# Performance work log

Measured on AMD Instinct MI355X. Metric: run time of the kernel, lower is better.

The kernel has to match this reference:

```python
import jax, jax.numpy as jnp
import numpy as np


def _edt(mask_zero):
    """Exact 2D Euclidean distance transform: distance of every pixel to the
    nearest True pixel in mask_zero (matches scipy.ndimage.distance_transform_edt
    applied to the one-hot map, where background pixels are zeros).
    mask_zero: [B, C, H, W] bool, True where the one-hot map is 0.
    Returns float32 [B, C, H, W].
    """
    B, C, H, W = mask_zero.shape
    BIG = jnp.float32(H + W)  # larger than any in-image 1D distance

    # Phase 1: 1D distance to nearest zero along axis H (forward + backward scans)
    def step(d, m):  # d,m: [B, C, W]
        d = jnp.where(m, 0.0, d + 1.0)
        return d, d

    m_rows = jnp.moveaxis(mask_zero, 2, 0)  # [H, B, C, W]
    init = jnp.full((B, C, W), BIG, dtype=jnp.float32)
    _, g_f = jax.lax.scan(step, init, m_rows)
    _, g_b = jax.lax.scan(step, init, m_rows[::-1])
    g = jnp.minimum(g_f, g_b[::-1])          # [H, B, C, W]
    g = jnp.moveaxis(g, 0, 2)                # [B, C, H, W]

    # Phase 2: exact combine along axis W: d2[.., i, j] = min_k g[.., i, k]^2 + (j-k)^2
    j = jnp.arange(W, dtype=jnp.float32)
    sq = (j[:, None] - j[None, :]) ** 2      # [W(j), W(k)]
    d2 = jnp.min(g[..., None, :] ** 2 + sq, axis=-1)  # [B, C, H, W]
    return jnp.sqrt(d2)


def _rrwmap(y_, num_classes):
    labels = y_[:, 0]  # [B, H, W]
    # one-hot channel c is zero where label != c
    mask_zero = labels[:, None, :, :] != jnp.arange(num_classes)[None, :, None, None]
    d = _edt(mask_zero)                                  # [B, C, H, W]
    maxd = jnp.max(d, axis=(2, 3), keepdims=True)        # per (b, c) max
    rrw = -(d / (maxd + 1e-15))
    return jnp.where(rrw == 0.0, 1.0, rrw)


def setup_inputs() -> dict:
    key = jax.random.key(0)
    k1, k2 = jax.random.split(key)
    B, C, H, W = 2, 4, 256, 256
    x = jax.random.normal(k1, (B, C, H, W), dtype=jnp.float32)
    y_ = jax.random.randint(k2, (B, 1, H, W), 0, C, dtype=jnp.int64)
    return {"x": x, "y_": y_}


def reference(x, y_):
    C = x.shape[1]
    rrw = _rrwmap(y_, C)
    p = jax.nn.softmax(x, axis=1)
    return jnp.mean(p * rrw)
```

## Files before the change

kernel.cpp:

```cpp
#include <hip/hip_runtime.h>

#define B_ 2
#define C_ 4
#define H_ 256
#define W_ 256
constexpr int BC    = B_ * C_;
constexpr int HW    = H_ * W_;
constexpr int NROWS = B_ * H_;
constexpr int NTOT  = B_ * C_ * HW;
constexpr float BIGF = (float)(H_ + W_);
constexpr int PF    = 6;

__global__ __launch_bounds__(256) void rows_kernel(
    const int* __restrict__ lab, const float* __restrict__ x,
    float* __restrict__ ps4, float* __restrict__ pm4, float* __restrict__ pa) {
    const int r = blockIdx.x;
    const int b = r >> 8;
    const int i = r & (H_ - 1);
    const int j = threadIdx.x;

    const int* lrow = lab + b * HW + i * W_;
    const int  c    = lrow[j];

    const float* xp = x + b * C_ * HW + i * W_ + j;
    const float x0 = xp[0 * HW], x1 = xp[1 * HW], x2 = xp[2 * HW], x3 = xp[3 * HW];

    const int* lcol = lab + b * HW + j;
    int lu[PF + 1], ld[PF + 1];
    #pragma unroll
    for (int k = 1; k <= PF; ++k) {
        const int ru = i - k, rd = i + k;
        lu[k] = lcol[(ru >= 0 ? ru : 0) * W_];
        ld[k] = lcol[(rd < H_ ? rd : H_ - 1) * W_];
    }
    float gu = -1.0f, gd = -1.0f;
    #pragma unroll
    for (int k = 1; k <= PF; ++k) {
        if (gu < 0.0f) {
            if (i - k < 0) gu = BIGF + (float)(i + 1);
            else if (lu[k] != c) gu = (float)k;
        }
        if (gd < 0.0f) {
            if (i + k >= H_) gd = BIGF + (float)(H_ - i);
            else if (ld[k] != c) gd = (float)k;
        }
    }
    for (int k = PF + 1; gu < 0.0f || gd < 0.0f; ++k) {
        if (gu < 0.0f) {
            const int rr = i - k;
            if (rr < 0) gu = BIGF + (float)(i + 1);
            else if (lcol[rr * W_] != c) gu = (float)k;
        }
        if (gd < 0.0f) {
            const int rr = i + k;
            if (rr >= H_) gd = BIGF + (float)(H_ - i);
            else if (lcol[rr * W_] != c) gd = (float)k;
        }
    }
    const float g = fminf(gu, gd);

    __shared__ int   ls[W_];
    __shared__ float g2s[W_];
    ls[j]  = c;
    g2s[j] = g * g;
    __syncthreads();

    float best = g * g;
    for (int dj = 1; dj < W_; ++dj) {
        const float dd = (float)(dj * dj);
        if (dd >= best) break;
        const int l = j - dj, rr = j + dj;
        if (l >= 0) {
            const float v = (ls[l] == c ? g2s[l] : 0.0f) + dd;
            best = fminf(best, v);
        }
        if (rr < W_) {
            const float v = (ls[rr] == c ? g2s[rr] : 0.0f) + dd;
            best = fminf(best, v);
        }
    }

    const float mx = fmaxf(fmaxf(x0, x1), fmaxf(x2, x3));
    const float e0 = __expf(x0 - mx), e1 = __expf(x1 - mx);
    const float e2 = __expf(x2 - mx), e3 = __expf(x3 - mx);
    const float s  = e0 + e1 + e2 + e3;
    const float ec = (c == 0) ? e0 : (c == 1) ? e1 : (c == 2) ? e2 : e3;
    const float pc = ec / s;

    float va = (s - ec) / s;
    const float psv = pc * sqrtf(best);
    float s0 = (c == 0) ? psv : 0.0f, s1 = (c == 1) ? psv : 0.0f;
    float s2 = (c == 2) ? psv : 0.0f, s3 = (c == 3) ? psv : 0.0f;
    float m0 = (c == 0) ? best : 0.0f, m1 = (c == 1) ? best : 0.0f;
    float m2 = (c == 2) ? best : 0.0f, m3 = (c == 3) ? best : 0.0f;

    #pragma unroll
    for (int off = 32; off; off >>= 1) {
        va += __shfl_down(va, off, 64);
        s0 += __shfl_down(s0, off, 64);
        s1 += __shfl_down(s1, off, 64);
        s2 += __shfl_down(s2, off, 64);
        s3 += __shfl_down(s3, off, 64);
        m0 = fmaxf(m0, __shfl_down(m0, off, 64));
        m1 = fmaxf(m1, __shfl_down(m1, off, 64));
        m2 = fmaxf(m2, __shfl_down(m2, off, 64));
        m3 = fmaxf(m3, __shfl_down(m3, off, 64));
    }
    __shared__ float lred[4][9];
    const int lane = j & 63, wid = j >> 6;
    if (lane == 0) {
        lred[wid][0] = va;
        lred[wid][1] = s0; lred[wid][2] = s1; lred[wid][3] = s2; lred[wid][4] = s3;
        lred[wid][5] = m0; lred[wid][6] = m1; lred[wid][7] = m2; lred[wid][8] = m3;
    }
    __syncthreads();
    if (j == 0) {
        float A = 0.0f, S0 = 0.0f, S1 = 0.0f, S2 = 0.0f, S3 = 0.0f;
        float M0 = 0.0f, M1 = 0.0f, M2 = 0.0f, M3 = 0.0f;
        #pragma unroll
        for (int w = 0; w < 4; ++w) {
            A  += lred[w][0];
            S0 += lred[w][1]; S1 += lred[w][2]; S2 += lred[w][3]; S3 += lred[w][4];
            M0 = fmaxf(M0, lred[w][5]); M1 = fmaxf(M1, lred[w][6]);
            M2 = fmaxf(M2, lred[w][7]); M3 = fmaxf(M3, lred[w][8]);
        }
        ((float4*)ps4)[r] = make_float4(S0, S1, S2, S3);
        ((float4*)pm4)[r] = make_float4(M0, M1, M2, M3);
        pa[r] = A;
    }
}

__global__ __launch_bounds__(64) void final_kernel(
    const float4* __restrict__ ps4, const float4* __restrict__ pm4,
    const float* __restrict__ pa, float* __restrict__ out) {
    const int t = threadIdx.x;
    float a = 0.0f;
    float4 sb0 = make_float4(0.f, 0.f, 0.f, 0.f), sb1 = sb0;
    float4 mb0 = sb0, mb1 = sb0;
    #pragma unroll
    for (int q = 0; q < 4; ++q) {
        const int r0 = t + q * 64;
        const int r1 = r0 + 256;
        a += pa[r0] + pa[r1];
        float4 v;
        v = ps4[r0]; sb0.x += v.x; sb0.y += v.y; sb0.z += v.z; sb0.w += v.w;
        v = ps4[r1]; sb1.x += v.x; sb1.y += v.y; sb1.z += v.z; sb1.w += v.w;
        v = pm4[r0]; mb0.x = fmaxf(mb0.x, v.x); mb0.y = fmaxf(mb0.y, v.y);
                     mb0.z = fmaxf(mb0.z, v.z); mb0.w = fmaxf(mb0.w, v.w);
        v = pm4[r1]; mb1.x = fmaxf(mb1.x, v.x); mb1.y = fmaxf(mb1.y, v.y);
                     mb1.z = fmaxf(mb1.z, v.z); mb1.w = fmaxf(mb1.w, v.w);
    }
    #pragma unroll
    for (int off = 32; off; off >>= 1) {
        a     += __shfl_down(a, off, 64);
        sb0.x += __shfl_down(sb0.x, off, 64); sb0.y += __shfl_down(sb0.y, off, 64);
        sb0.z += __shfl_down(sb0.z, off, 64); sb0.w += __shfl_down(sb0.w, off, 64);
        sb1.x += __shfl_down(sb1.x, off, 64); sb1.y += __shfl_down(sb1.y, off, 64);
        sb1.z += __shfl_down(sb1.z, off, 64); sb1.w += __shfl_down(sb1.w, off, 64);
        mb0.x = fmaxf(mb0.x, __shfl_down(mb0.x, off, 64));
        mb0.y = fmaxf(mb0.y, __shfl_down(mb0.y, off, 64));
        mb0.z = fmaxf(mb0.z, __shfl_down(mb0.z, off, 64));
        mb0.w = fmaxf(mb0.w, __shfl_down(mb0.w, off, 64));
        mb1.x = fmaxf(mb1.x, __shfl_down(mb1.x, off, 64));
        mb1.y = fmaxf(mb1.y, __shfl_down(mb1.y, off, 64));
        mb1.z = fmaxf(mb1.z, __shfl_down(mb1.z, off, 64));
        mb1.w = fmaxf(mb1.w, __shfl_down(mb1.w, off, 64));
    }
    if (t == 0) {
        float total = a;
        total -= sb0.x / (sqrtf(mb0.x) + 1e-15f);
        total -= sb0.y / (sqrtf(mb0.y) + 1e-15f);
        total -= sb0.z / (sqrtf(mb0.z) + 1e-15f);
        total -= sb0.w / (sqrtf(mb0.w) + 1e-15f);
        total -= sb1.x / (sqrtf(mb1.x) + 1e-15f);
        total -= sb1.y / (sqrtf(mb1.y) + 1e-15f);
        total -= sb1.z / (sqrtf(mb1.z) + 1e-15f);
        total -= sb1.w / (sqrtf(mb1.w) + 1e-15f);
        out[0] = total / (float)NTOT;
    }
}

extern "C" void kernel_launch(void* const* d_in, const int* in_sizes, int n_in,
                              void* d_out, int out_size, void* d_ws, size_t ws_size,
                              hipStream_t stream) {
    const float* x = (const float*)d_in[0];
    const int*   y = (const int*)d_in[1];
    float* out = (float*)d_out;

    float* ps4 = (float*)d_ws;
    float* pm4 = ps4 + NROWS * 4;
    float* pa  = pm4 + NROWS * 4;

    rows_kernel<<<NROWS, W_, 0, stream>>>(y, x, ps4, pm4, pa);
    final_kernel<<<1, 64, 0, stream>>>((const float4*)ps4, (const float4*)pm4, pa, out);
}
```

Before: 61.72 us.

## Process four pixels per thread with vectorized int4/float4 loads, single-wavefront blocks

Each block now uses one 64-lane wavefront, and each thread handles four adjacent columns using int4/float4 loads for labels and logits. Because the block is a single wavefront, the cross-wave shared-memory reduction and its second barrier go away. The prefetch depth for the vertical scan grows from 6 to 8 rows. The trade-off is less parallelism: four times fewer threads overall, and each thread runs four serial horizontal EDT searches plus four vertical fallback loops, which adds latency and divergence.

```diff
diff --git a/kernel.cpp b/kernel.cpp
--- a/kernel.cpp
+++ b/kernel.cpp
@@ -9,90 +9,124 @@
 constexpr int NROWS = B_ * H_;
 constexpr int NTOT  = B_ * C_ * HW;
 constexpr float BIGF = (float)(H_ + W_);
-constexpr int PF    = 6;
-
-__global__ __launch_bounds__(256) void rows_kernel(
+constexpr int PF    = 8;
+
+__device__ __forceinline__ int   icomp(const int4& v, int p) {
+    return p == 0 ? v.x : p == 1 ? v.y : p == 2 ? v.z : v.w;
+}
+__device__ __forceinline__ float fcomp(const float4& v, int p) {
+    return p == 0 ? v.x : p == 1 ? v.y : p == 2 ? v.z : v.w;
+}
+
+__global__ __launch_bounds__(64) void rows_kernel(
     const int* __restrict__ lab, const float* __restrict__ x,
     float* __restrict__ ps4, float* __restrict__ pm4, float* __restrict__ pa) {
     const int r = blockIdx.x;
     const int b = r >> 8;
     const int i = r & (H_ - 1);
-    const int j = threadIdx.x;
-
-    const int* lrow = lab + b * HW + i * W_;
-    const int  c    = lrow[j];
-
-    const float* xp = x + b * C_ * HW + i * W_ + j;
-    const float x0 = xp[0 * HW], x1 = xp[1 * HW], x2 = xp[2 * HW], x3 = xp[3 * HW];
-
-    const int* lcol = lab + b * HW + j;
-    int lu[PF + 1], ld[PF + 1];
+    const int t = threadIdx.x;
+
+    const int4* lrowv = (const int4*)(lab + b * HW + i * W_);
+    const int4  L     = lrowv[t];
+
+    const float4* xv = (const float4*)(x + b * C_ * HW + i * W_) + t;
+    const float4 X0 = xv[0 * (HW / 4)], X1 = xv[1 * (HW / 4)];
+    const float4 X2 = xv[2 * (HW / 4)], X3 = xv[3 * (HW / 4)];
+
+    const int4* lcolv = (const int4*)(lab + b * HW) + t;
+    int4 lu[PF + 1], ld[PF + 1];
     #pragma unroll
     for (int k = 1; k <= PF; ++k) {
         const int ru = i - k, rd = i + k;
-        lu[k] = lcol[(ru >= 0 ? ru : 0) * W_];
-        ld[k] = lcol[(rd < H_ ? rd : H_ - 1) * W_];
-    }
-    float gu = -1.0f, gd = -1.0f;
+        lu[k] = lcolv[(ru >= 0 ? ru : 0) * (W_ / 4)];
+        ld[k] = lcolv[(rd < H_ ? rd : H_ - 1) * (W_ / 4)];
+    }
+
+    float gu[4], gd[4];
+    #pragma unroll
+    for (int p = 0; p < 4; ++p) { gu[p] = -1.0f; gd[p] = -1.0f; }
     #pragma unroll
     for (int k = 1; k <= PF; ++k) {
-        if (gu < 0.0f) {
-            if (i - k < 0) gu = BIGF + (float)(i + 1);
-            else if (lu[k] != c) gu = (float)k;
-        }
-        if (gd < 0.0f) {
-            if (i + k >= H_) gd = BIGF + (float)(H_ - i);
-            else if (ld[k] != c) gd = (float)k;
-        }
-    }
-    for (int k = PF + 1; gu < 0.0f || gd < 0.0f; ++k) {
-        if (gu < 0.0f) {
+        #pragma unroll
+        for (int p = 0; p < 4; ++p) {
+            const int cp = icomp(L, p);
+            if (gu[p] < 0.0f) {
+                if (i - k < 0) gu[p] = BIGF + (float)(i + 1);
+                else if (icomp(lu[k], p) != cp) gu[p] = (float)k;
+            }
+            if (gd[p] < 0.0f) {
+                if (i + k >= H_) gd[p] = BIGF + (float)(H_ - i);
+                else if (icomp(ld[k], p) != cp) gd[p] = (float)k;
+            }
+        }
+    }
+    #pragma unroll
+    for (int p = 0; p < 4; ++p) {
+        const int* lcolp = lab + b * HW + 4 * t + p;
+        const int  cp    = icomp(L, p);
+        for (int k = PF + 1; gu[p] < 0.0f; ++k) {
             const int rr = i - k;
-            if (rr < 0) gu = BIGF + (float)(i + 1);
-            else if (lcol[rr * W_] != c) gu = (float)k;
-        }
-        if (gd < 0.0f) {
+            if (rr < 0) gu[p] = BIGF + (float)(i + 1);
+            else if (lcolp[rr * W_] != cp) gu[p] = (float)k;
+        }
+        for (int k = PF + 1; gd[p] < 0.0f; ++k) {
             const int rr = i + k;
-            if (rr >= H_) gd = BIGF + (float)(H_ - i);
-            else if (lcol[rr * W_] != c) gd = (float)k;
-        }
-    }
-    const float g = fminf(gu, gd);
-
-    __shared__ int   ls[W_];
-    __shared__ float g2s[W_];
-    ls[j]  = c;
-    g2s[j] = g * g;
+            if (rr >= H_) gd[p] = BIGF + (float)(H_ - i);
+            else if (lcolp[rr * W_] != cp) gd[p] = (float)k;
+        }
+    }
+
+    __shared__ alignas(16) int   ls[W_];
+    __shared__ alignas(16) float g2s[W_];
+    float g2[4];
+    #pragma unroll
+    for (int p = 0; p < 4; ++p) {
+        const float g = fminf(gu[p], gd[p]);
+        g2[p] = g * g;
+    }
+    ((int4*)ls)[t]    = L;
+    ((float4*)g2s)[t] = make_float4(g2[0], g2[1], g2[2], g2[3]);
     __syncthreads();
 
-    float best = g * g;
-    for (int dj = 1; dj < W_; ++dj) {
-        const float dd = (float)(dj * dj);
-        if (dd >= best) break;
-        const int l = j - dj, rr = j + dj;
-        if (l >= 0) {
-            const float v = (ls[l] == c ? g2s[l] : 0.0f) + dd;
-            best = fminf(best, v);
-        }
-        if (rr < W_) {
-            const float v = (ls[rr] == c ? g2s[rr] : 0.0f) + dd;
-            best = fminf(best, v);
-        }
-    }
-
-    const float mx = fmaxf(fmaxf(x0, x1), fmaxf(x2, x3));
-    const float e0 = __expf(x0 - mx), e1 = __expf(x1 - mx);
-    const float e2 = __expf(x2 - mx), e3 = __expf(x3 - mx);
-    const float s  = e0 + e1 + e2 + e3;
-    const float ec = (c == 0) ? e0 : (c == 1) ? e1 : (c == 2) ? e2 : e3;
-    const float pc = ec / s;
-
-    float va = (s - ec) / s;
-    const float psv = pc * sqrtf(best);
-    float s0 = (c == 0) ? psv : 0.0f, s1 = (c == 1) ? psv : 0.0f;
-    float s2 = (c == 2) ? psv : 0.0f, s3 = (c == 3) ? psv : 0.0f;
-    float m0 = (c == 0) ? best : 0.0f, m1 = (c == 1) ? best : 0.0f;
-    float m2 = (c == 2) ? best : 0.0f, m3 = (c == 3) ? best : 0.0f;
+    float best[4];
+    #pragma unroll
+    for (int p = 0; p < 4; ++p) {
+        const int j  = 4 * t + p;
+        const int cp = icomp(L, p);
+        float bb = g2[p];
+        for (int dj = 1; dj < W_; ++dj) {
+            const float dd = (float)(dj * dj);
+            if (dd >= bb) break;
+            const int l = j - dj, rr = j + dj;
+            if (l >= 0)  bb = fminf(bb, (ls[l] == cp ? g2s[l] : 0.0f) + dd);
+            if (rr < W_) bb = fminf(bb, (ls[rr] == cp ? g2s[rr] : 0.0f) + dd);
+        }
+        best[p] = bb;
+    }
+
+    float va = 0.0f;
+    float s0 = 0.0f, s1 = 0.0f, s2 = 0.0f, s3 = 0.0f;
+    float m0 = 0.0f, m1 = 0.0f, m2 = 0.0f, m3 = 0.0f;
+    #pragma unroll
+    for (int p = 0; p < 4; ++p) {
+        const float x0 = fcomp(X0, p), x1 = fcomp(X1, p);
+        const float x2 = fcomp(X2, p), x3 = fcomp(X3, p);
+        const float mx = fmaxf(fmaxf(x0, x1), fmaxf(x2, x3));
+        const float e0 = __expf(x0 - mx), e1 = __expf(x1 - mx);
+        const float e2 = __expf(x2 - mx), e3 = __expf(x3 - mx);
+        const float s  = e0 + e1 + e2 + e3;
+        const int   cp = icomp(L, p);
+        const float ec = (cp == 0) ? e0 : (cp == 1) ? e1 : (cp == 2) ? e2 : e3;
+        const float pc = ec / s;
+        va += (s - ec) / s;
+        const float psv = pc * sqrtf(best[p]);
+        s0 += (cp == 0) ? psv : 0.0f; s1 += (cp == 1) ? psv : 0.0f;
+        s2 += (cp == 2) ? psv : 0.0f; s3 += (cp == 3) ? psv : 0.0f;
+        m0 = fmaxf(m0, (cp == 0) ? best[p] : 0.0f);
+        m1 = fmaxf(m1, (cp == 1) ? best[p] : 0.0f);
+        m2 = fmaxf(m2, (cp == 2) ? best[p] : 0.0f);
+        m3 = fmaxf(m3, (cp == 3) ? best[p] : 0.0f);
+    }
 
     #pragma unroll
     for (int off = 32; off; off >>= 1) {
@@ -106,27 +140,10 @@
         m2 = fmaxf(m2, __shfl_down(m2, off, 64));
         m3 = fmaxf(m3, __shfl_down(m3, off, 64));
     }
-    __shared__ float lred[4][9];
-    const int lane = j & 63, wid = j >> 6;
-    if (lane == 0) {
-        lred[wid][0] = va;
-        lred[wid][1] = s0; lred[wid][2] = s1; lred[wid][3] = s2; lred[wid][4] = s3;
-        lred[wid][5] = m0; lred[wid][6] = m1; lred[wid][7] = m2; lred[wid][8] = m3;
-    }
-    __syncthreads();
-    if (j == 0) {
-        float A = 0.0f, S0 = 0.0f, S1 = 0.0f, S2 = 0.0f, S3 = 0.0f;
-        float M0 = 0.0f, M1 = 0.0f, M2 = 0.0f, M3 = 0.0f;
-        #pragma unroll
-        for (int w = 0; w < 4; ++w) {
-            A  += lred[w][0];
-            S0 += lred[w][1]; S1 += lred[w][2]; S2 += lred[w][3]; S3 += lred[w][4];
-            M0 = fmaxf(M0, lred[w][5]); M1 = fmaxf(M1, lred[w][6]);
-            M2 = fmaxf(M2, lred[w][7]); M3 = fmaxf(M3, lred[w][8]);
-        }
-        ((float4*)ps4)[r] = make_float4(S0, S1, S2, S3);
-        ((float4*)pm4)[r] = make_float4(M0, M1, M2, M3);
-        pa[r] = A;
+    if (t == 0) {
+        ((float4*)ps4)[r] = make_float4(s0, s1, s2, s3);
+        ((float4*)pm4)[r] = make_float4(m0, m1, m2, m3);
+        pa[r] = va;
     }
 }
 
@@ -191,6 +208,6 @@
     float* pm4 = ps4 + NROWS * 4;
     float* pa  = pm4 + NROWS * 4;
 
-    rows_kernel<<<NROWS, W_, 0, stream>>>(y, x, ps4, pm4, pa);
+    rows_kernel<<<NROWS, 64, 0, stream>>>(y, x, ps4, pm4, pa);
     final_kernel<<<1, 64, 0, stream>>>((const float4*)ps4, (const float4*)pm4, pa, out);
 }
```

Result: slower. 64.70 us (+4.8%).
